# Optimization experiments

Hardware: AMD Instinct MI355X
Metric: run time of the kernel (lower is better)

Reference implementation:

```python
import jax, jax.numpy as jnp
import numpy as np

B, C, OC, H, W = 2, 64, 128, 96, 96
HD, DI, N, R, K = C // 2, C, 16, 2, 4  # VSSBlock: hidden=C/2, d_inner=2*hidden=C, d_state, dt_rank, 4 scan dirs
EPS = 1e-5


def _conv(x, w, b, pad, groups=1):
    y = jax.lax.conv_general_dilated(x, w, (1, 1), pad, feature_group_count=groups,
                                     dimension_numbers=('NCHW', 'OIHW', 'NCHW'))
    return y + b[None, :, None, None]


def _ln(x, w, b):
    m = x.mean(-1, keepdims=True)
    v = x.var(-1, keepdims=True)
    return (x - m) * jax.lax.rsqrt(v + EPS) * w + b


def _selective_scan(xs, dts, Bs, Cs, A, D):
    # xs, dts: (B,K,DI,L); Bs, Cs: (B,K,N,L); A: (K,DI,N); D: (K,DI)
    dts = jax.nn.softplus(dts)

    def step(h, inp):
        u_t, dt_t, B_t, C_t = inp
        dA = jnp.exp(dt_t[..., None] * A)                         # (B,K,DI,N)
        h = dA * h + (dt_t * u_t)[..., None] * B_t[:, :, None, :]
        return h, jnp.einsum('bkdn,bkn->bkd', h, C_t)

    seq = (jnp.moveaxis(xs, -1, 0), jnp.moveaxis(dts, -1, 0),
           jnp.moveaxis(Bs, -1, 0), jnp.moveaxis(Cs, -1, 0))
    h0 = jnp.zeros(xs.shape[:3] + (A.shape[-1],), xs.dtype)
    _, ys = jax.lax.scan(step, h0, seq)
    return jnp.moveaxis(ys, 0, -1) + D[None, :, :, None] * xs


def _vss_block(x, ln_w, ln_b, in_w, conv_w, conv_b, xproj_w, dtproj_w, dtproj_b,
               A_logs, Ds, on_w, on_b, out_w):
    # x: (B,H,W,HD); VMamba SS2D with 4-direction cross-scan + residual
    b, hh, ww, _ = x.shape
    L = hh * ww
    h = _ln(x, ln_w, ln_b)
    xz = h @ in_w                                   # (B,H,W,2*DI)
    xp, z = jnp.split(xz, 2, axis=-1)
    xc = jnp.transpose(xp, (0, 3, 1, 2))            # (B,DI,H,W)
    xc = jax.nn.silu(_conv(xc, conv_w, conv_b, ((1, 1), (1, 1)), groups=DI))
    x_flat = xc.reshape(b, DI, L)
    x_wh = jnp.transpose(xc, (0, 1, 3, 2)).reshape(b, DI, L)
    x2 = jnp.stack([x_flat, x_wh], axis=1)
    xs = jnp.concatenate([x2, jnp.flip(x2, -1)], axis=1)      # (B,4,DI,L)
    x_dbl = jnp.einsum('bkdl,kcd->bkcl', xs, xproj_w)
    dts, Bs, Cs = jnp.split(x_dbl, [R, R + N], axis=2)
    dts = jnp.einsum('bkrl,kdr->bkdl', dts, dtproj_w) + dtproj_b[None, :, :, None]
    A = -jnp.exp(A_logs)
    ys = _selective_scan(xs, dts, Bs, Cs, A, Ds)              # (B,4,DI,L)
    inv = jnp.flip(ys[:, 2:4], -1)
    unwh = lambda t: jnp.transpose(t.reshape(b, DI, ww, hh), (0, 1, 3, 2)).reshape(b, DI, L)
    y = ys[:, 0] + inv[:, 0] + unwh(ys[:, 1]) + unwh(inv[:, 1])
    y = jnp.transpose(y.reshape(b, DI, hh, ww), (0, 2, 3, 1))
    y = _ln(y, on_w, on_b) * jax.nn.silu(z)
    return x + y @ out_w


def _forward(x, ms_dw33_w, ms_dw33_b, ms_in_w, ms_in_b, ms_scale,
             vss_ln_w, vss_ln_b, vss_in_w, vss_conv_w, vss_conv_b, vss_xproj_w,
             vss_dtproj_w, vss_dtproj_b, vss_A_logs, vss_Ds, vss_on_w, vss_on_b, vss_out_w,
             ma_conv_w, ma_conv_b, adw_h_w, adw_h_b, adw_w_w, adw_w_b,
             pw_w, pw_b, bn_w, bn_b, bn_mean, bn_var):
    vss = (vss_ln_w, vss_ln_b, vss_in_w, vss_conv_w, vss_conv_b, vss_xproj_w,
           vss_dtproj_w, vss_dtproj_b, vss_A_logs, vss_Ds, vss_on_w, vss_on_b, vss_out_w)
    # --- MambaSplit (shared VSSBlock applied to both channel halves) ---
    xd = _conv(x, ms_dw33_w, ms_dw33_b, ((1, 1), (1, 1)), groups=C)
    x1, x2 = jnp.split(xd, 2, axis=1)

    def branch(xp):
        y = _vss_block(jnp.transpose(xp, (0, 2, 3, 1)), *vss)
        return ms_scale * xp + jnp.transpose(y, (0, 3, 1, 2))

    xm = jnp.concatenate([branch(x1), branch(x2)], axis=1)
    m = xm.mean((2, 3), keepdims=True)
    v = xm.var((2, 3), keepdims=True)
    xm = (xm - m) * jax.lax.rsqrt(v + EPS) * ms_in_w[None, :, None, None] + ms_in_b[None, :, None, None]
    xm = jax.nn.leaky_relu(xm, 0.01)
    # --- MaxAvg (global avg+max pool -> 3x3 conv on 1x1 map -> sigmoid gate) ---
    pooled = jnp.concatenate([x.mean((2, 3), keepdims=True), x.max((2, 3), keepdims=True)], axis=1)
    gate = jax.nn.sigmoid(_conv(pooled, ma_conv_w, ma_conv_b, ((1, 1), (1, 1))))
    xs_ = xm + gate * x
    # --- AxialDW ---
    xs_ = xs_ + _conv(xs_, adw_h_w, adw_h_b, ((1, 1), (0, 0)), groups=C) \
              + _conv(xs_, adw_w_w, adw_w_b, ((0, 0), (1, 1)), groups=C)
    # --- BN (eval) + ReLU, 1x1 conv, 2x2 maxpool ---
    skip = jax.nn.relu((xs_ - bn_mean[None, :, None, None]) * jax.lax.rsqrt(bn_var[None, :, None, None] + EPS)
                       * bn_w[None, :, None, None] + bn_b[None, :, None, None])
    out = _conv(skip, pw_w, pw_b, ((0, 0), (0, 0)))
    down = jax.lax.reduce_window(out, -jnp.inf, jax.lax.max, (1, 1, 2, 2), (1, 1, 2, 2), 'VALID')
    return down, skip


def setup_inputs() -> dict:
    key = jax.random.key(0)
    ks = jax.random.split(key, 16)
    r = lambda i, shape, s=0.02: jax.random.normal(ks[i], shape, jnp.float32) * s
    return {
        'x': jax.random.normal(ks[0], (B, C, H, W), jnp.float32),
        'ms_dw33_w': r(1, (C, 1, 3, 3), 0.1), 'ms_dw33_b': jnp.zeros(C),
        'ms_in_w': jnp.ones(C), 'ms_in_b': jnp.zeros(C),
        'ms_scale': jnp.ones((1,)),
        'vss_ln_w': jnp.ones(HD), 'vss_ln_b': jnp.zeros(HD),
        'vss_in_w': r(2, (HD, 2 * DI)),
        'vss_conv_w': r(3, (DI, 1, 3, 3), 0.1), 'vss_conv_b': jnp.zeros(DI),
        'vss_xproj_w': r(4, (K, R + 2 * N, DI)),
        'vss_dtproj_w': r(5, (K, DI, R), 0.1), 'vss_dtproj_b': r(6, (K, DI), 0.1),
        'vss_A_logs': jnp.tile(jnp.log(jnp.arange(1, N + 1, dtype=jnp.float32)), (K, DI, 1)),
        'vss_Ds': jnp.ones((K, DI)),
        'vss_on_w': jnp.ones(DI), 'vss_on_b': jnp.zeros(DI),
        'vss_out_w': r(7, (DI, HD)),
        'ma_conv_w': r(8, (C, 2 * C, 3, 3), 0.05), 'ma_conv_b': jnp.zeros(C),
        'adw_h_w': r(9, (C, 1, 3, 1), 0.1), 'adw_h_b': jnp.zeros(C),
        'adw_w_w': r(10, (C, 1, 1, 3), 0.1), 'adw_w_b': jnp.zeros(C),
        'pw_w': r(11, (OC, C, 1, 1)), 'pw_b': jnp.zeros(OC),
        'bn_w': jnp.ones(C), 'bn_b': jnp.zeros(C),
        'bn_mean': jnp.zeros(C), 'bn_var': jnp.ones(C),
    }


def reference(x, ms_dw33_w, ms_dw33_b, ms_in_w, ms_in_b, ms_scale,
              vss_ln_w, vss_ln_b, vss_in_w, vss_conv_w, vss_conv_b, vss_xproj_w,
              vss_dtproj_w, vss_dtproj_b, vss_A_logs, vss_Ds, vss_on_w, vss_on_b, vss_out_w,
              ma_conv_w, ma_conv_b, adw_h_w, adw_h_b, adw_w_w, adw_w_b,
              pw_w, pw_b, bn_w, bn_b, bn_mean, bn_var):
    return _forward(x, ms_dw33_w, ms_dw33_b, ms_in_w, ms_in_b, ms_scale,
                    vss_ln_w, vss_ln_b, vss_in_w, vss_conv_w, vss_conv_b, vss_xproj_w,
                    vss_dtproj_w, vss_dtproj_b, vss_A_logs, vss_Ds, vss_on_w, vss_on_b, vss_out_w,
                    ma_conv_w, ma_conv_b, adw_h_w, adw_h_b, adw_w_w, adw_w_b,
                    pw_w, pw_b, bn_w, bn_b, bn_mean, bn_var)
```

## Files before the change

### kernel.cpp

```cpp
#include <hip/hip_runtime.h>
#include <hip/hip_bf16.h>

typedef __hip_bfloat16 bf16;
#define DEV __device__ __forceinline__

constexpr int B_ = 2, C_ = 64, H_ = 96, W_ = 96, L_ = 9216;
constexpr int HD_ = 32, DI_ = 64, N_ = 16, K_ = 4, BB_ = 4;
constexpr int OC_ = 128;
constexpr int CH_ = 768, CL_ = 12;
constexpr int SEGN = 16, SEGC = 48;
constexpr float EPSF = 1e-5f;
constexpr int DOWN_SZ = B_ * OC_ * 48 * 48;

typedef __attribute__((ext_vector_type(8))) short short8;
typedef __attribute__((ext_vector_type(4))) float f32x4;

DEV float softplusf(float x) { return x > 15.f ? x : __logf(1.f + __expf(x)); }
DEV float b2f(bf16 v) { return __bfloat162float(v); }
DEV float lo16f(unsigned v) { return __uint_as_float(v << 16); }
DEV float hi16f(unsigned v) { return __uint_as_float(v & 0xffff0000u); }
DEV void unpk(uint4 a, uint4 b, float* v) {
  v[0] = lo16f(a.x); v[1] = hi16f(a.x); v[2] = lo16f(a.y); v[3] = hi16f(a.y);
  v[4] = lo16f(a.z); v[5] = hi16f(a.z); v[6] = lo16f(a.w); v[7] = hi16f(a.w);
  v[8] = lo16f(b.x); v[9] = hi16f(b.x); v[10] = lo16f(b.y); v[11] = hi16f(b.y);
  v[12] = lo16f(b.z); v[13] = hi16f(b.z); v[14] = lo16f(b.w); v[15] = hi16f(b.w);
}

__constant__ float kLogN[16] = {
  0.0f, 0.69314718f, 1.09861229f, 1.38629436f, 1.60943791f, 1.79175947f,
  1.94591015f, 2.07944154f, 2.19722458f, 2.30258509f, 2.39789527f,
  2.48490665f, 2.56494936f, 2.63905733f, 2.70805020f, 2.77258872f};

DEV void pow_tree(float e1, float* ep) {
  float e2 = e1 * e1, e4 = e2 * e2, e8 = e4 * e4;
  float e3 = e2 * e1, e5 = e4 * e1, e6 = e4 * e2, e7 = e4 * e3;
  ep[0] = e1;  ep[1] = e2;  ep[2] = e3;  ep[3] = e4;
  ep[4] = e5;  ep[5] = e6;  ep[6] = e7;  ep[7] = e8;
  ep[8] = e8 * e1;  ep[9] = e8 * e2;  ep[10] = e8 * e3;  ep[11] = e8 * e4;
  ep[12] = e8 * e5; ep[13] = e8 * e6; ep[14] = e8 * e7;  ep[15] = e8 * e8;
}

DEV void ld_bu(const float* __restrict__ bB, const bf16* __restrict__ ub, int d,
               int ls, int uidx, uint4& qb0, uint4& qb1, float& t0, float& t1, float& u) {
  int uls = __builtin_amdgcn_readfirstlane(ls);
  const float* p = bB + (size_t)uls * 12;
  qb0 = *(const uint4*)p; qb1 = *(const uint4*)(p + 4);
  t0 = p[8]; t1 = p[9];
  u = b2f(ub[(size_t)uidx * DI_ + d]);
}
DEV void ld_bcu(const float* __restrict__ bB, const bf16* __restrict__ bC,
                const bf16* __restrict__ ub, int d, int ls, int uidx,
                uint4& qb0, uint4& qb1, uint4& qc0, uint4& qc1,
                float& t0, float& t1, float& u) {
  int uls = __builtin_amdgcn_readfirstlane(ls);
  const float* p = bB + (size_t)uls * 12;
  qb0 = *(const uint4*)p; qb1 = *(const uint4*)(p + 4);
  t0 = p[8]; t1 = p[9];
  const uint4* cq = (const uint4*)(bC + (size_t)uls * 16);
  qc0 = cq[0]; qc1 = cq[1];
  u = b2f(ub[(size_t)uidx * DI_ + d]);
}

__global__ __launch_bounds__(256, 4) void k_front(
    const float* __restrict__ x, const float* __restrict__ dw33w,
    const float* __restrict__ dw33b, const float* __restrict__ lnw,
    const float* __restrict__ lnb, const float* __restrict__ inw,
    const float* __restrict__ xpw, const float* __restrict__ alog,
    float* __restrict__ xd, float* __restrict__ xzA, bf16* __restrict__ xzBh,
    bf16* __restrict__ wh, float* __restrict__ aux) {
  int bb = blockIdx.y, t = threadIdx.x;
  int b = bb & 1, co = (bb >> 1) * HD_;
  int idx0 = blockIdx.x * 64;
  if (bb == 0) {
    int i = blockIdx.x * 256 + t;
    if (i < 144 * 64) {
      int n = i >> 6;
      wh[i] = __float2bfloat16(n < 136 ? xpw[i] : 0.f);
    }
    if (blockIdx.x == 0) {
      int kd = t;
      const float* al = alog + kd * N_;
      float a0 = al[0];
      bool lin = true;
#pragma unroll
      for (int n = 1; n < N_; n++) lin = lin && (fabsf(al[n] - a0 - kLogN[n]) < 3e-5f);
      aux[kd] = -__expf(a0);
      aux[256 + kd] = lin ? 1.f : 0.f;
#pragma unroll
      for (int n = 0; n < N_; n++) aux[512 + kd * N_ + n] = -__expf(al[n]);
    }
  }
  __shared__ float xds[32 * 68];
  __shared__ float meanA[64], rstdA[64];
  for (int i = t; i < 2048; i += 256) {
    int cl = i >> 6, ii = i & 63;
    int sp = idx0 + ii, wi = sp % 96, hi = sp / 96;
    int cg = b * C_ + co + cl;
    float acc = dw33b[co + cl];
#pragma unroll
    for (int dy = -1; dy <= 1; dy++) {
      int hh = hi + dy; if (hh < 0 || hh >= H_) continue;
#pragma unroll
      for (int dx = -1; dx <= 1; dx++) {
        int ww = wi + dx; if (ww < 0 || ww >= W_) continue;
        acc = fmaf(x[(size_t)cg * L_ + sp + dy * 96 + dx],
                   dw33w[(co + cl) * 9 + (dy + 1) * 3 + (dx + 1)], acc);
      }
    }
    xds[cl * 68 + ii] = acc;
    xd[(size_t)cg * L_ + sp] = acc;
  }
  __syncthreads();
  if (t < 64) {
    float s = 0.f, sq = 0.f;
#pragma unroll
    for (int c = 0; c < 32; c++) { float v = xds[c * 68 + t]; s += v; sq = fmaf(v, v, sq); }
    float mean = s * (1.f / HD_);
    float var = sq * (1.f / HD_) - mean * mean;
    meanA[t] = mean; rstdA[t] = rsqrtf(var + EPSF);
  }
  __syncthreads();
  for (int i = t; i < 2048; i += 256) {
    int c = i >> 6, idx = i & 63;
    float v = xds[c * 68 + idx];
    xds[c * 68 + idx] = (v - meanA[idx]) * rstdA[idx] * lnw[c] + lnb[c];
  }
  __syncthreads();
  int oc = t & 127, g = t >> 7;
  float acc[32];
#pragma unroll
  for (int j = 0; j < 32; j++) acc[j] = 0.f;
  for (int c = 0; c < 32; c++) {
    float wv = inw[c * 128 + oc];
    const float4* row = reinterpret_cast<const float4*>(&xds[c * 68 + g * 32]);
#pragma unroll
    for (int j4 = 0; j4 < 8; j4++) {
      float4 xv = row[j4];
      acc[j4 * 4 + 0] = fmaf(xv.x, wv, acc[j4 * 4 + 0]);
      acc[j4 * 4 + 1] = fmaf(xv.y, wv, acc[j4 * 4 + 1]);
      acc[j4 * 4 + 2] = fmaf(xv.z, wv, acc[j4 * 4 + 2]);
      acc[j4 * 4 + 3] = fmaf(xv.w, wv, acc[j4 * 4 + 3]);
    }
  }
  int occ = oc & 63;
  if (oc < 64) {
#pragma unroll
    for (int j = 0; j < 32; j++)
      xzA[(size_t)(bb * L_ + idx0 + g * 32 + j) * 64 + occ] = acc[j];
  } else {
#pragma unroll
    for (int j = 0; j < 32; j++)
      xzBh[(size_t)(bb * L_ + idx0 + g * 32 + j) * 64 + occ] = __float2bfloat16(acc[j]);
  }
}

__global__ void k_dwsilu(const float* __restrict__ xzA, const float* __restrict__ cw,
                         const float* __restrict__ cb, bf16* __restrict__ xch,
                         bf16* __restrict__ xcht) {
  int t = blockIdx.x * 256 + threadIdx.x;
  int d = t & 63, idx = (t >> 6) % L_, bb = t / (L_ * DI_);
  int wi = idx % W_, hi = idx / W_;
  float acc = cb[d];
#pragma unroll
  for (int dy = -1; dy <= 1; dy++) {
    int hh = hi + dy; if (hh < 0 || hh >= H_) continue;
#pragma unroll
    for (int dx = -1; dx <= 1; dx++) {
      int ww = wi + dx; if (ww < 0 || ww >= W_) continue;
      acc = fmaf(xzA[(size_t)(bb * L_ + hh * W_ + ww) * 64 + d],
                 cw[d * 9 + (dy + 1) * 3 + (dx + 1)], acc);
    }
  }
  acc = acc / (1.f + __expf(-acc));
  bf16 v = __float2bfloat16(acc);
  xch[t] = v;
  int idx_t = wi * 96 + hi;
  xcht[((size_t)bb * L_ + idx_t) * DI_ + d] = v;
}

__global__ __launch_bounds__(256, 4) void k_xdbl_mfma(
    const bf16* __restrict__ xch, const bf16* __restrict__ wh,
    float* __restrict__ xdblB, bf16* __restrict__ xdblC) {
  int w = threadIdx.x >> 6, lane = threadIdx.x & 63;
  int bb = blockIdx.y;
  int mtile = blockIdx.x * 4 + w;
  int idx0 = mtile * 16;
  int m = lane & 15, quad = lane >> 4;
  const bf16* arow = xch + ((size_t)bb * L_ + idx0 + m) * 64 + quad * 8;
  short8 a0 = *reinterpret_cast<const short8*>(arow);
  short8 a1 = *reinterpret_cast<const short8*>(arow + 32);
#pragma unroll
  for (int nt = 0; nt < 9; nt++) {
    int n = nt * 16 + m;
    const bf16* brow = wh + n * 64 + quad * 8;
    short8 b0 = *reinterpret_cast<const short8*>(brow);
    short8 b1 = *reinterpret_cast<const short8*>(brow + 32);
    f32x4 acc = {0.f, 0.f, 0.f, 0.f};
    acc = __builtin_amdgcn_mfma_f32_16x16x32_bf16(a0, b0, acc, 0, 0, 0);
    acc = __builtin_amdgcn_mfma_f32_16x16x32_bf16(a1, b1, acc, 0, 0, 0);
    if (n < 136) {
      int k4 = (n >= 102) ? 3 : (n >= 68) ? 2 : (n >= 34) ? 1 : 0;
      int c = n - k4 * 34;
#pragma unroll
      for (int i = 0; i < 4; i++) {
        int r = idx0 + quad * 4 + i;
        int hi2 = r / 96, wi2 = r - hi2 * 96;
        int tr = wi2 * 96 + hi2;
        int ls = (k4 == 0) ? r : (k4 == 1) ? tr : (k4 == 2) ? (L_ - 1 - r) : (L_ - 1 - tr);
        size_t row = (size_t)(bb * K_ + k4) * L_ + ls;
        if (c < 2)       xdblB[row * 12 + 8 + c] = acc[i];
        else if (c < 18) ((bf16*)(xdblB + row * 12))[c - 2] = __float2bfloat16(acc[i]);
        else             xdblC[row * 16 + (c - 18)] = __float2bfloat16(acc[i]);
      }
    }
  }
}

__global__ __launch_bounds__(256, 4) void k_scan1(
    const float* __restrict__ xdblB, const bf16* __restrict__ xch,
    const bf16* __restrict__ xcht, const float* __restrict__ dtw,
    const float* __restrict__ dtb, const float* __restrict__ aux,
    bf16* __restrict__ hbuf, float* __restrict__ ssum) {
  int w = threadIdx.x >> 6, d = threadIdx.x & 63;
  int chunk = blockIdx.x * 4 + w, k = blockIdx.y, bb = blockIdx.z;
  float w0 = dtw[(k * DI_ + d) * 2 + 0], w1 = dtw[(k * DI_ + d) * 2 + 1];
  float bia = dtb[k * DI_ + d];
  float A1 = aux[k * 64 + d];
  bool chain = (__ballot(aux[256 + k * 64 + d] > 0.5f) == ~0ull);
  float h[N_];
#pragma unroll
  for (int n = 0; n < N_; n++) h[n] = 0.f;
  const float* bB = xdblB + (size_t)(bb * K_ + k) * L_ * 12;
  const bf16* ub = ((k & 1) ? xcht : xch) + (size_t)bb * L_ * DI_;
  int ls0 = chunk * CL_;
  int uidx0 = (k & 2) ? (L_ - 1 - ls0) : ls0;
  int ustep = (k & 2) ? -1 : 1;
  float S = 0.f;
  if (chain) {
#pragma unroll 2
    for (int s = 0; s < CL_; s++) {
      uint4 qb0, qb1; float t0, t1, u;
      ld_bu(bB, ub, d, ls0 + s, uidx0 + s * ustep, qb0, qb1, t0, t1, u);
      float Bv[16];
      unpk(qb0, qb1, Bv);
      float dt = softplusf(fmaf(t0, w0, fmaf(t1, w1, bia)));
      S += dt;
      float du = dt * u;
      float ep[16];
      pow_tree(__expf(dt * A1), ep);
#pragma unroll
      for (int n = 0; n < N_; n++) h[n] = fmaf(ep[n], h[n], du * Bv[n]);
    }
  } else {
    float A[N_];
#pragma unroll
    for (int n = 0; n < N_; n++) A[n] = aux[512 + (k * 64 + d) * N_ + n];
    for (int s = 0; s < CL_; s++) {
      uint4 qb0, qb1; float t0, t1, u;
      ld_bu(bB, ub, d, ls0 + s, uidx0 + s * ustep, qb0, qb1, t0, t1, u);
      float Bv[16];
      unpk(qb0, qb1, Bv);
      float dt = softplusf(fmaf(t0, w0, fmaf(t1, w1, bia)));
      S += dt;
      float du = dt * u;
#pragma unroll
      for (int n = 0; n < N_; n++) h[n] = fmaf(__expf(dt * A[n]), h[n], du * Bv[n]);
    }
  }
  size_t base = (size_t)((bb * K_ + k) * CH_ + chunk) * DI_ + d;
  ssum[base] = S;
#pragma unroll
  for (int n = 0; n < N_; n++) hbuf[base * N_ + n] = __float2bfloat16(h[n]);
}

__global__ __launch_bounds__(256, 4) void k_scan2a(
    const float* __restrict__ aux, const float* __restrict__ ssum,
    bf16* __restrict__ hbuf, float* __restrict__ cumS,
    float* __restrict__ segH, float* __restrict__ segS) {
  int t = blockIdx.x * 256 + threadIdx.x;
  int n = t & 15, d = (t >> 4) & 63, kk = (t >> 10) & 3, bb = (t >> 12) & 3, seg = t >> 14;
  float A = aux[512 + (kk * 64 + d) * N_ + n];
  size_t row = (size_t)(bb * K_ + kk) * CH_ * DI_ + d;
  float hp = 0.f, Sc = 0.f;
#pragma unroll 4
  for (int j = 0; j < SEGC; j++) {
    int c = seg * SEGC + j;
    size_t sb = row + (size_t)c * DI_;
    float S = ssum[sb];
    float hl = b2f(hbuf[sb * N_ + n]);
    hbuf[sb * N_ + n] = __float2bfloat16(hp);
    if (n == 0) cumS[sb] = Sc;
    hp = fmaf(__expf(A * S), hp, hl);
    Sc += S;
  }
  size_t sbase = (size_t)(bb * K_ + kk) * SEGN + seg;
  segH[(sbase * DI_ + d) * N_ + n] = hp;
  if (n == 0) segS[sbase * DI_ + d] = Sc;
}

__global__ __launch_bounds__(256, 4) void k_scan3(
    const float* __restrict__ xdblB, const bf16* __restrict__ xdblC,
    const bf16* __restrict__ xch, const bf16* __restrict__ xcht,
    const float* __restrict__ dtw, const float* __restrict__ dtb,
    const float* __restrict__ Dsw, const float* __restrict__ aux,
    const bf16* __restrict__ hbuf, const float* __restrict__ cumS,
    const float* __restrict__ segH, const float* __restrict__ segS,
    bf16* __restrict__ ydir) {
  int w = threadIdx.x >> 6, d = threadIdx.x & 63;
  int chunk = blockIdx.x * 4 + w, k = blockIdx.y, bb = blockIdx.z;
  float w0 = dtw[(k * DI_ + d) * 2 + 0], w1 = dtw[(k * DI_ + d) * 2 + 1];
  float bia = dtb[k * DI_ + d];
  float Dk = Dsw[k * DI_ + d];
  float A1 = aux[k * 64 + d];
  bool chain = (__ballot(aux[256 + k * 64 + d] > 0.5f) == ~0ull);
  float A[N_];
  if (!chain) {
#pragma unroll
    for (int n = 0; n < N_; n++) A[n] = aux[512 + (k * 64 + d) * N_ + n];
  }
  int seg = chunk / SEGC;
  float Hi[N_];
#pragma unroll
  for (int n = 0; n < N_; n++) Hi[n] = 0.f;
  for (int s = 0; s < seg; s++) {
    size_t sb = (size_t)(bb * K_ + k) * SEGN + s;
    float Ssg = segS[sb * DI_ + d];
    const float* Hs = segH + (sb * DI_ + d) * N_;
    if (chain) {
      float ep[16];
      pow_tree(__expf(A1 * Ssg), ep);
#pragma unroll
      for (int n = 0; n < N_; n++) Hi[n] = fmaf(ep[n], Hi[n], Hs[n]);
    } else {
#pragma unroll
      for (int n = 0; n < N_; n++) Hi[n] = fmaf(__expf(A[n] * Ssg), Hi[n], Hs[n]);
    }
  }
  float h[N_];
  size_t base = (size_t)((bb * K_ + k) * CH_ + chunk) * DI_ + d;
  float Sc = cumS[base];
  {
    const bf16* hb = hbuf + base * N_;
    uint4 qh0 = *(const uint4*)hb, qh1 = *(const uint4*)(hb + 8);
    unpk(qh0, qh1, h);
    if (chain) {
      float ep[16];
      pow_tree(__expf(A1 * Sc), ep);
#pragma unroll
      for (int n = 0; n < N_; n++) h[n] = fmaf(ep[n], Hi[n], h[n]);
    } else {
#pragma unroll
      for (int n = 0; n < N_; n++) h[n] = fmaf(__expf(A[n] * Sc), Hi[n], h[n]);
    }
  }
  const float* bB = xdblB + (size_t)(bb * K_ + k) * L_ * 12;
  const bf16* bC = xdblC + (size_t)(bb * K_ + k) * L_ * 16;
  const bf16* ub = ((k & 1) ? xcht : xch) + (size_t)bb * L_ * DI_;
  bf16* yb = ydir + (size_t)(bb * K_ + k) * L_ * DI_;
  int ls0 = chunk * CL_;
  int uidx0 = (k & 2) ? (L_ - 1 - ls0) : ls0;
  int ustep = (k & 2) ? -1 : 1;
  if (chain) {
#pragma unroll 2
    for (int s = 0; s < CL_; s++) {
      uint4 qb0, qb1, qc0, qc1; float t0, t1, u;
      ld_bcu(bB, bC, ub, d, ls0 + s, uidx0 + s * ustep, qb0, qb1, qc0, qc1, t0, t1, u);
      float Bv[16], Cv[16];
      unpk(qb0, qb1, Bv); unpk(qc0, qc1, Cv);
      float dt = softplusf(fmaf(t0, w0, fmaf(t1, w1, bia)));
      float du = dt * u;
      float ep[16];
      pow_tree(__expf(dt * A1), ep);
      float m[16];
#pragma unroll
      for (int n = 0; n < N_; n++) {
        h[n] = fmaf(ep[n], h[n], du * Bv[n]);
        m[n] = h[n] * Cv[n];
      }
      float a0 = m[0] + m[1], a1 = m[2] + m[3], a2 = m[4] + m[5], a3 = m[6] + m[7];
      float a4 = m[8] + m[9], a5 = m[10] + m[11], a6 = m[12] + m[13], a7 = m[14] + m[15];
      float b0 = a0 + a1, b1 = a2 + a3, b2 = a4 + a5, b3 = a6 + a7;
      float y = fmaf(Dk, u, (b0 + b1) + (b2 + b3));
      yb[(size_t)(ls0 + s) * DI_ + d] = __float2bfloat16(y);
    }
  } else {
    for (int s = 0; s < CL_; s++) {
      uint4 qb0, qb1, qc0, qc1; float t0, t1, u;
      ld_bcu(bB, bC, ub, d, ls0 + s, uidx0 + s * ustep, qb0, qb1, qc0, qc1, t0, t1, u);
      float Bv[16], Cv[16];
      unpk(qb0, qb1, Bv); unpk(qc0, qc1, Cv);
      float dt = softplusf(fmaf(t0, w0, fmaf(t1, w1, bia)));
      float du = dt * u;
      float y = 0.f;
#pragma unroll
      for (int n = 0; n < N_; n++) {
        h[n] = fmaf(__expf(dt * A[n]), h[n], du * Bv[n]);
        y = fmaf(h[n], Cv[n], y);
      }
      y = fmaf(Dk, u, y);
      yb[(size_t)(ls0 + s) * DI_ + d] = __float2bfloat16(y);
    }
  }
}

__global__ void k_combine(const bf16* __restrict__ ydir, const bf16* __restrict__ xzBh,
                          const float* __restrict__ xd, const float* __restrict__ onw,
                          const float* __restrict__ onb, const float* __restrict__ outw,
                          const float* __restrict__ mssc, float* __restrict__ xm) {
  int w = threadIdx.x >> 6, d = threadIdx.x & 63;
  int idx = blockIdx.x * 4 + w, bb = blockIdx.y;
  int b = bb & 1, co = (bb >> 1) * HD_;
  int hii = idx / 96, wii = idx - hii * 96;
  int lt = wii * 96 + hii;
  const bf16* yd = ydir + (size_t)bb * K_ * L_ * DI_;
  float y = b2f(yd[((size_t)0 * L_ + idx) * DI_ + d])
          + b2f(yd[((size_t)1 * L_ + lt) * DI_ + d])
          + b2f(yd[((size_t)2 * L_ + (L_ - 1 - idx)) * DI_ + d])
          + b2f(yd[((size_t)3 * L_ + (L_ - 1 - lt)) * DI_ + d]);
  float s = y, sq = y * y;
#pragma unroll
  for (int m = 1; m < 64; m <<= 1) { s += __shfl_xor(s, m, 64); sq += __shfl_xor(sq, m, 64); }
  float mean = s * (1.f / DI_);
  float var = sq * (1.f / DI_) - mean * mean;
  float rstd = rsqrtf(var + EPSF);
  float yn = (y - mean) * rstd * onw[d] + onb[d];
  float z = b2f(xzBh[(size_t)(bb * L_ + idx) * 64 + d]);
  float g = yn * (z / (1.f + __expf(-z)));
  __shared__ float gs[4][DI_];
  gs[w][d] = g;
  __syncthreads();
  if (d < HD_) {
    float acc = 0.f;
#pragma unroll
    for (int dd = 0; dd < DI_; dd++) acc = fmaf(gs[w][dd], outw[dd * HD_ + d], acc);
    size_t xi = (size_t)(b * C_ + co + d) * L_ + idx;
    float xp = xd[xi];
    xm[xi] = mssc[0] * xp + xp + acc;
  }
}

__global__ __launch_bounds__(1024) void k_stats(
    const float* __restrict__ xm, const float* __restrict__ x,
    float* __restrict__ inm, float* __restrict__ inr,
    float* __restrict__ xmean, float* __restrict__ xmax) {
  int bc = blockIdx.x, t = threadIdx.x;
  const float* pm = xm + (size_t)bc * L_;
  const float* px = x + (size_t)bc * L_;
  float s = 0.f, sq = 0.f, xs = 0.f, mx = -1e30f;
  for (int i = t; i < L_; i += 1024) {
    float v = pm[i]; s += v; sq = fmaf(v, v, sq);
    float xv = px[i]; xs += xv; mx = fmaxf(mx, xv);
  }
  __shared__ float red[64];
#pragma unroll
  for (int m = 1; m < 64; m <<= 1) {
    s += __shfl_xor(s, m, 64); sq += __shfl_xor(sq, m, 64);
    xs += __shfl_xor(xs, m, 64); mx = fmaxf(mx, __shfl_xor(mx, m, 64));
  }
  int wid = t >> 6;
  if ((t & 63) == 0) { red[wid] = s; red[16 + wid] = sq; red[32 + wid] = xs; red[48 + wid] = mx; }
  __syncthreads();
  if (t == 0) {
    s = 0.f; sq = 0.f; xs = 0.f; mx = -1e30f;
#pragma unroll
    for (int i = 0; i < 16; i++) {
      s += red[i]; sq += red[16 + i]; xs += red[32 + i]; mx = fmaxf(mx, red[48 + i]);
    }
    float mean = s * (1.f / L_);
    float var = sq * (1.f / L_) - mean * mean;
    inm[bc] = mean;
    inr[bc] = rsqrtf(var + EPSF);
    xmean[bc] = xs * (1.f / L_);
    xmax[bc] = mx;
  }
}

__global__ void k_axbn(const float* __restrict__ xm, const float* __restrict__ x,
                       const float* __restrict__ inm, const float* __restrict__ inr,
                       const float* __restrict__ msw, const float* __restrict__ msb,
                       const float* __restrict__ xmean, const float* __restrict__ xmax,
                       const float* __restrict__ maw, const float* __restrict__ mab,
                       const float* __restrict__ hw, const float* __restrict__ hb,
                       const float* __restrict__ wwt, const float* __restrict__ wb,
                       const float* __restrict__ bnw, const float* __restrict__ bnb,
                       const float* __restrict__ bnm, const float* __restrict__ bnv,
                       float* __restrict__ skipo) {
  int t = blockIdx.x * 256 + threadIdx.x;
  int bc = t / L_, c = bc & 63, b = bc >> 6;
  __shared__ float gsh;
  if (threadIdx.x < 64) {
    int ic = threadIdx.x;
    float p = xmean[b * 64 + ic] * maw[(c * 128 + ic) * 9 + 4]
            + xmax[b * 64 + ic] * maw[(c * 128 + 64 + ic) * 9 + 4];
#pragma unroll
    for (int m = 1; m < 64; m <<= 1) p += __shfl_xor(p, m, 64);
    if (ic == 0) gsh = 1.f / (1.f + __expf(-(p + mab[c])));
  }
  __syncthreads();
  float gate = gsh, im = inm[bc], ir = inr[bc], mw = msw[c], mb = msb[c];
  int wi = t % W_, hi = (t / W_) % H_;
  auto xsv = [&](int tt) -> float {
    float v = xm[tt];
    v = (v - im) * ir * mw + mb;
    v = v > 0.f ? v : 0.01f * v;
    return v + gate * x[tt];
  };
  float a = xsv(t);
  float hacc = hb[c];
#pragma unroll
  for (int dy = -1; dy <= 1; dy++) {
    int hh = hi + dy; if (hh < 0 || hh >= H_) continue;
    hacc = fmaf(xsv(t + dy * W_), hw[c * 3 + dy + 1], hacc);
  }
  float wacc = wb[c];
#pragma unroll
  for (int dx = -1; dx <= 1; dx++) {
    int ww = wi + dx; if (ww < 0 || ww >= W_) continue;
    wacc = fmaf(xsv(t + dx), wwt[c * 3 + dx + 1], wacc);
  }
  float v = a + hacc + wacc;
  float sv = (v - bnm[c]) * rsqrtf(bnv[c] + EPSF) * bnw[c] + bnb[c];
  skipo[t] = fmaxf(sv, 0.f);
}

__global__ void k_pwpool(const float* __restrict__ skipo, const float* __restrict__ pww,
                         const float* __restrict__ pwb, float* __restrict__ down) {
  int h2 = blockIdx.x, b = blockIdx.y, t = threadIdx.x;
  int oc0 = blockIdx.z * 32;
  __shared__ float sk[64 * 192];
  for (int i = t; i < 64 * 192; i += 256) {
    int c = i / 192, rw = i % 192, r = rw / 96, wcol = rw % 96;
    sk[i] = skipo[((size_t)(b * C_ + c) * H_ + (2 * h2 + r)) * W_ + wcol];
  }
  __syncthreads();
  for (int o = t; o < 32 * 48; o += 256) {
    int oc = oc0 + o / 48, w2 = o % 48;
    float s0 = 0.f, s1 = 0.f, s2 = 0.f, s3 = 0.f;
#pragma unroll 8
    for (int c = 0; c < 64; c++) {
      float wv = pww[oc * 64 + c];
      const float* sp = &sk[c * 192 + 2 * w2];
      s0 = fmaf(sp[0], wv, s0);
      s1 = fmaf(sp[1], wv, s1);
      s2 = fmaf(sp[96], wv, s2);
      s3 = fmaf(sp[97], wv, s3);
    }
    float v = fmaxf(fmaxf(s0, s1), fmaxf(s2, s3)) + pwb[oc];
    down[((size_t)(b * OC_ + oc) * 48 + h2) * 48 + w2] = v;
  }
}

extern "C" void kernel_launch(void* const* d_in, const int* in_sizes, int n_in,
                              void* d_out, int out_size, void* d_ws, size_t ws_size,
                              hipStream_t stream) {
  const float* x     = (const float*)d_in[0];
  const float* dw33w = (const float*)d_in[1];
  const float* dw33b = (const float*)d_in[2];
  const float* msw   = (const float*)d_in[3];
  const float* msb   = (const float*)d_in[4];
  const float* mssc  = (const float*)d_in[5];
  const float* lnw   = (const float*)d_in[6];
  const float* lnb   = (const float*)d_in[7];
  const float* inw   = (const float*)d_in[8];
  const float* cw    = (const float*)d_in[9];
  const float* cb    = (const float*)d_in[10];
  const float* xpw   = (const float*)d_in[11];
  const float* dtw   = (const float*)d_in[12];
  const float* dtb   = (const float*)d_in[13];
  const float* alog  = (const float*)d_in[14];
  const float* Dsw   = (const float*)d_in[15];
  const float* onw   = (const float*)d_in[16];
  const float* onb   = (const float*)d_in[17];
  const float* outw  = (const float*)d_in[18];
  const float* maw   = (const float*)d_in[19];
  const float* mab   = (const float*)d_in[20];
  const float* ahw   = (const float*)d_in[21];
  const float* ahb   = (const float*)d_in[22];
  const float* aww   = (const float*)d_in[23];
  const float* awb   = (const float*)d_in[24];
  const float* pww   = (const float*)d_in[25];
  const float* pwb   = (const float*)d_in[26];
  const float* bnw   = (const float*)d_in[27];
  const float* bnb   = (const float*)d_in[28];
  const float* bnm   = (const float*)d_in[29];
  const float* bnv   = (const float*)d_in[30];

  float* ws = (float*)d_ws;
  float* xd    = ws;
  float* hreg  = xd + 1179648;
  bf16*  hbuf  = (bf16*)hreg;
  float* xzA   = hreg;
  bf16*  xzBh  = (bf16*)(hreg + 6291456);
  float* xdblB = hreg + 6291456 + 1179648;
  bf16*  xdblC = (bf16*)(xdblB + 1769472);
  float* ssum  = xdblB + 1769472 + 1179648;
  bf16*  ydir  = (bf16*)(ssum + 786432);
  float* xmR   = ssum + 786432 + 4718592;
  bf16*  xch   = (bf16*)xmR;
  float* xm    = xmR;
  float* st    = xmR + 1179648;
  float* inm = st, *inr = st + 128, *xmean = st + 256, *xmaxv = st + 384;
  float* aux   = st + 512;
  bf16*  wh    = (bf16*)(aux + 4608);
  float* cumS  = aux + 4608 + 4608;
  float* segH  = cumS + 786432;
  float* segS  = segH + 262144;
  bf16*  xcht  = (bf16*)(segS + 16384);

  float* outp = (float*)d_out;
  float* down = outp;
  float* skipo = outp + DOWN_SZ;

  dim3 b256(256);
  int nEl = B_ * C_ * L_;

  k_front<<<dim3(L_ / 64, BB_), b256, 0, stream>>>(x, dw33w, dw33b, lnw, lnb, inw,
                                                   xpw, alog, xd, xzA, xzBh, wh, aux);
  k_dwsilu<<<dim3(BB_ * L_ * DI_ / 256), b256, 0, stream>>>(xzA, cw, cb, xch, xcht);
  k_xdbl_mfma<<<dim3(L_ / 64, BB_), b256, 0, stream>>>(xch, wh, xdblB, xdblC);
  k_scan1<<<dim3(CH_ / 4, K_, BB_), b256, 0, stream>>>(xdblB, xch, xcht, dtw, dtb, aux, hbuf, ssum);
  k_scan2a<<<dim3(BB_ * K_ * SEGN * DI_ * N_ / 256), b256, 0, stream>>>(aux, ssum, hbuf, cumS, segH, segS);
  k_scan3<<<dim3(CH_ / 4, K_, BB_), b256, 0, stream>>>(xdblB, xdblC, xch, xcht, dtw, dtb, Dsw,
                                                      aux, hbuf, cumS, segH, segS, ydir);
  k_combine<<<dim3(L_ / 4, BB_), b256, 0, stream>>>(ydir, xzBh, xd, onw, onb, outw, mssc, xm);
  k_stats<<<dim3(B_ * C_), dim3(1024), 0, stream>>>(xm, x, inm, inr, xmean, xmaxv);
  k_axbn<<<dim3((nEl + 255) / 256), b256, 0, stream>>>(xm, x, inm, inr, msw, msb, xmean, xmaxv,
                                                      maw, mab, ahw, ahb, aww, awb,
                                                      bnw, bnb, bnm, bnv, skipo);
  k_pwpool<<<dim3(48, B_, 4), b256, 0, stream>>>(skipo, pww, pwb, down);
}
```

Baseline: 343.7 us.

## Precompute segment carry-in states in a separate scan pass

```diff
diff --git a/kernel.cpp b/kernel.cpp
--- a/kernel.cpp
+++ b/kernel.cpp
@@ -298,14 +298,29 @@
   if (n == 0) segS[sbase * DI_ + d] = Sc;
 }
 
+__global__ void k_scan2b(const float* __restrict__ aux, float* __restrict__ segH,
+                         const float* __restrict__ segS) {
+  int t = blockIdx.x * 256 + threadIdx.x;
+  int n = t & 15, d = (t >> 4) & 63, kk = (t >> 10) & 3, bb = t >> 12;
+  float A = aux[512 + (kk * 64 + d) * N_ + n];
+  float hp = 0.f;
+  for (int seg = 0; seg < SEGN; seg++) {
+    size_t sbase = (size_t)(bb * K_ + kk) * SEGN + seg;
+    size_t si = (sbase * DI_ + d) * N_ + n;
+    float H = segH[si];
+    float E = __expf(A * segS[sbase * DI_ + d]);
+    segH[si] = hp;
+    hp = fmaf(E, hp, H);
+  }
+}
+
 __global__ __launch_bounds__(256, 4) void k_scan3(
     const float* __restrict__ xdblB, const bf16* __restrict__ xdblC,
     const bf16* __restrict__ xch, const bf16* __restrict__ xcht,
     const float* __restrict__ dtw, const float* __restrict__ dtb,
     const float* __restrict__ Dsw, const float* __restrict__ aux,
     const bf16* __restrict__ hbuf, const float* __restrict__ cumS,
-    const float* __restrict__ segH, const float* __restrict__ segS,
-    bf16* __restrict__ ydir) {
+    const float* __restrict__ segH, bf16* __restrict__ ydir) {
   int w = threadIdx.x >> 6, d = threadIdx.x & 63;
   int chunk = blockIdx.x * 4 + w, k = blockIdx.y, bb = blockIdx.z;
   float w0 = dtw[(k * DI_ + d) * 2 + 0], w1 = dtw[(k * DI_ + d) * 2 + 1];
@@ -313,44 +328,27 @@
   float Dk = Dsw[k * DI_ + d];
   float A1 = aux[k * 64 + d];
   bool chain = (__ballot(aux[256 + k * 64 + d] > 0.5f) == ~0ull);
-  float A[N_];
-  if (!chain) {
-#pragma unroll
-    for (int n = 0; n < N_; n++) A[n] = aux[512 + (k * 64 + d) * N_ + n];
-  }
-  int seg = chunk / SEGC;
-  float Hi[N_];
-#pragma unroll
-  for (int n = 0; n < N_; n++) Hi[n] = 0.f;
-  for (int s = 0; s < seg; s++) {
-    size_t sb = (size_t)(bb * K_ + k) * SEGN + s;
-    float Ssg = segS[sb * DI_ + d];
-    const float* Hs = segH + (sb * DI_ + d) * N_;
-    if (chain) {
-      float ep[16];
-      pow_tree(__expf(A1 * Ssg), ep);
-#pragma unroll
-      for (int n = 0; n < N_; n++) Hi[n] = fmaf(ep[n], Hi[n], Hs[n]);
-    } else {
-#pragma unroll
-      for (int n = 0; n < N_; n++) Hi[n] = fmaf(__expf(A[n] * Ssg), Hi[n], Hs[n]);
-    }
-  }
   float h[N_];
   size_t base = (size_t)((bb * K_ + k) * CH_ + chunk) * DI_ + d;
+  int seg = chunk / SEGC;
+  size_t sbase = (size_t)(bb * K_ + k) * SEGN + seg;
   float Sc = cumS[base];
   {
     const bf16* hb = hbuf + base * N_;
     uint4 qh0 = *(const uint4*)hb, qh1 = *(const uint4*)(hb + 8);
     unpk(qh0, qh1, h);
+    const float* Hin = segH + (sbase * DI_ + d) * N_;
     if (chain) {
       float ep[16];
       pow_tree(__expf(A1 * Sc), ep);
 #pragma unroll
-      for (int n = 0; n < N_; n++) h[n] = fmaf(ep[n], Hi[n], h[n]);
+      for (int n = 0; n < N_; n++) h[n] = fmaf(ep[n], Hin[n], h[n]);
     } else {
 #pragma unroll
-      for (int n = 0; n < N_; n++) h[n] = fmaf(__expf(A[n] * Sc), Hi[n], h[n]);
+      for (int n = 0; n < N_; n++) {
+        float A = aux[512 + (k * 64 + d) * N_ + n];
+        h[n] = fmaf(__expf(A * Sc), Hin[n], h[n]);
+      }
     }
   }
   const float* bB = xdblB + (size_t)(bb * K_ + k) * L_ * 12;
@@ -384,6 +382,9 @@
       yb[(size_t)(ls0 + s) * DI_ + d] = __float2bfloat16(y);
     }
   } else {
+    float A[N_];
+#pragma unroll
+    for (int n = 0; n < N_; n++) A[n] = aux[512 + (k * 64 + d) * N_ + n];
     for (int s = 0; s < CL_; s++) {
       uint4 qb0, qb1, qc0, qc1; float t0, t1, u;
       ld_bcu(bB, bC, ub, d, ls0 + s, uidx0 + s * ustep, qb0, qb1, qc0, qc1, t0, t1, u);
@@ -620,8 +621,9 @@
   k_xdbl_mfma<<<dim3(L_ / 64, BB_), b256, 0, stream>>>(xch, wh, xdblB, xdblC);
   k_scan1<<<dim3(CH_ / 4, K_, BB_), b256, 0, stream>>>(xdblB, xch, xcht, dtw, dtb, aux, hbuf, ssum);
   k_scan2a<<<dim3(BB_ * K_ * SEGN * DI_ * N_ / 256), b256, 0, stream>>>(aux, ssum, hbuf, cumS, segH, segS);
+  k_scan2b<<<dim3(BB_ * K_ * DI_ * N_ / 256), b256, 0, stream>>>(aux, segH, segS);
   k_scan3<<<dim3(CH_ / 4, K_, BB_), b256, 0, stream>>>(xdblB, xdblC, xch, xcht, dtw, dtb, Dsw,
-                                                      aux, hbuf, cumS, segH, segS, ydir);
+                                                      aux, hbuf, cumS, segH, ydir);
   k_combine<<<dim3(L_ / 4, BB_), b256, 0, stream>>>(ydir, xzBh, xd, onw, onb, outw, mssc, xm);
   k_stats<<<dim3(B_ * C_), dim3(1024), 0, stream>>>(xm, x, inm, inr, xmean, xmaxv);
   k_axbn<<<dim3((nEl + 255) / 256), b256, 0, stream>>>(xm, x, inm, inr, msw, msb, xmean, xmaxv,
```

Measured after the change: 320.4 us. 6.8% less time.
